# Performance work log

Measured on AMD Instinct MI355X. Metric: run time of the kernel, lower is better.

Reference implementation:

```python
import jax, jax.numpy as jnp
import numpy as np

N_HEADS = 16
ROPE_BASE = 10000.0


def setup_inputs() -> dict:
    key = jax.random.key(0)
    k1, k2, k3 = jax.random.split(key, 3)
    B, L, D = 2, 2048, 2048
    x = jax.random.normal(k1, (B, L, D), dtype=jnp.float32)
    w_qkv = jax.random.normal(k2, (D, 3 * D), dtype=jnp.float32) * (1.0 / np.sqrt(D))
    w_out = jax.random.normal(k3, (D, D), dtype=jnp.float32) * (1.0 / np.sqrt(D))
    return {"x": x, "w_qkv": w_qkv, "w_out": w_out}


def _rope_cos_sin(L, head_dim, dtype):
    # inv_freq over even dims, freqs duplicated across both halves (HF convention)
    inv_freq = 1.0 / (ROPE_BASE ** (jnp.arange(0, head_dim, 2, dtype=jnp.float32) / head_dim))
    freqs = jnp.arange(L, dtype=jnp.float32)[:, None] * inv_freq[None, :]  # [L, hd/2]
    emb = jnp.concatenate([freqs, freqs], axis=-1)  # [L, hd]
    return jnp.cos(emb).astype(dtype), jnp.sin(emb).astype(dtype)


def _rotate_half(t):
    h = t.shape[-1] // 2
    return jnp.concatenate([-t[..., h:], t[..., :h]], axis=-1)


def reference(x, w_qkv, w_out):
    B, L, D = x.shape
    H = N_HEADS
    hd = D // H
    qkv = x @ w_qkv  # [B, L, 3D]
    q, k, v = jnp.split(qkv, 3, axis=-1)

    def heads(t):  # [B, L, D] -> [B, H, L, hd]
        return t.reshape(B, L, H, hd).transpose(0, 2, 1, 3)

    q, k, v = heads(q), heads(k), heads(v)
    cos, sin = _rope_cos_sin(L, hd, x.dtype)  # [L, hd] broadcast over B,H
    q = q * cos + _rotate_half(q) * sin
    k = k * cos + _rotate_half(k) * sin
    # SDPA, no mask, no dropout (eval), not causal
    scale = 1.0 / np.sqrt(hd)
    scores = jnp.einsum('bhld,bhsd->bhls', q, k) * scale
    attn = jax.nn.softmax(scores, axis=-1)
    y = jnp.einsum('bhls,bhsd->bhld', attn, v)  # [B, H, L, hd]
    y = y.transpose(0, 2, 1, 3).reshape(B, L, D)
    return y @ w_out
```

## Files before the change

kernel.cpp:

```cpp
#include <hip/hip_runtime.h>

typedef __attribute__((ext_vector_type(8))) short bf16x8;
typedef __attribute__((ext_vector_type(8))) unsigned short u16x8;
typedef __attribute__((ext_vector_type(4))) float f32x4;
typedef __attribute__((ext_vector_type(4))) unsigned short u16x4;

#define BB 2
#define LL 2048
#define DD 2048
#define HH 16
#define HDIM 128
#define MM 4096
#define NQKV 6144

__device__ __forceinline__ unsigned short f2bf(float f) {
    unsigned int u = __builtin_bit_cast(unsigned int, f);
    u += 0x7FFFu + ((u >> 16) & 1u);
    return (unsigned short)(u >> 16);
}
__device__ __forceinline__ float bf2f(unsigned short h) {
    unsigned int u = ((unsigned int)h) << 16;
    return __builtin_bit_cast(float, u);
}

__device__ __forceinline__ void gload16(const unsigned short* g, unsigned short* l) {
    __builtin_amdgcn_global_load_lds((const __attribute__((address_space(1))) void*)g,
                                     (__attribute__((address_space(3))) void*)l, 16, 0, 0);
}

__global__ __launch_bounds__(256) void k_cvt_bf16(const float* __restrict__ in,
                                                  unsigned short* __restrict__ out,
                                                  int n4) {
    int i = blockIdx.x * 256 + threadIdx.x;
    if (i < n4) {
        float4 v = reinterpret_cast<const float4*>(in)[i];
        u16x4 o;
        o[0] = f2bf(v.x); o[1] = f2bf(v.y); o[2] = f2bf(v.z); o[3] = f2bf(v.w);
        reinterpret_cast<u16x4*>(out)[i] = o;
    }
}

__global__ __launch_bounds__(256) void k_cvt_T(const float* __restrict__ in,
                                               unsigned short* __restrict__ out,
                                               int K, int N) {
    __shared__ unsigned short t[64][72];
    int n0 = blockIdx.x * 64, k0 = blockIdx.y * 64;
    int tid = threadIdx.x;
    int tr = tid >> 4, tc = tid & 15;
    #pragma unroll
    for (int i = 0; i < 4; ++i) {
        int k = i * 16 + tr;
        float4 v = *reinterpret_cast<const float4*>(in + (size_t)(k0 + k) * N + n0 + tc * 4);
        t[tc * 4 + 0][k] = f2bf(v.x);
        t[tc * 4 + 1][k] = f2bf(v.y);
        t[tc * 4 + 2][k] = f2bf(v.z);
        t[tc * 4 + 3][k] = f2bf(v.w);
    }
    __syncthreads();
    #pragma unroll
    for (int i = 0; i < 4; ++i) {
        int n = i * 16 + tr;
        u16x4 o = *reinterpret_cast<u16x4*>(&t[n][tc * 4]);
        *reinterpret_cast<u16x4*>(out + (size_t)(n0 + n) * K + k0 + tc * 4) = o;
    }
}

__global__ __launch_bounds__(256) void k_transV(const unsigned short* __restrict__ in,
                                                unsigned short* __restrict__ out) {
    __shared__ unsigned short t[64][68];
    int l0 = blockIdx.x * 64, d0 = blockIdx.y * 64;
    int bh = blockIdx.z;
    const unsigned short* ib = in + (size_t)bh * LL * HDIM;
    unsigned short* ob = out + (size_t)bh * HDIM * LL;
    int tid = threadIdx.x;
    int tr = tid >> 4, tc = tid & 15;
    #pragma unroll
    for (int i = 0; i < 4; ++i) {
        int l = i * 16 + tr;
        u16x4 v = *reinterpret_cast<const u16x4*>(ib + (size_t)(l0 + l) * HDIM + d0 + tc * 4);
        t[tc * 4 + 0][l] = v[0];
        t[tc * 4 + 1][l] = v[1];
        t[tc * 4 + 2][l] = v[2];
        t[tc * 4 + 3][l] = v[3];
    }
    __syncthreads();
    #pragma unroll
    for (int i = 0; i < 4; ++i) {
        int d = i * 16 + tr;
        u16x4 o = *reinterpret_cast<u16x4*>(&t[d][tc * 4]);
        *reinterpret_cast<u16x4*>(ob + (size_t)(d0 + d) * LL + l0 + tc * 4) = o;
    }
}

__global__ __launch_bounds__(256) void k_rope_table(float* __restrict__ ct,
                                                    float* __restrict__ st) {
    int idx = blockIdx.x * 256 + threadIdx.x;
    if (idx >= LL * 64) return;
    int pos = idx >> 6, d = idx & 63;
    float freq = __expf(-(float)d * (9.210340371976184f / 64.0f));
    float ang = (float)pos * freq;
    ct[idx] = cosf(ang);
    st[idx] = sinf(ang);
}

__global__ __launch_bounds__(256) void k_rope_apply(unsigned short* __restrict__ Q,
                                                    unsigned short* __restrict__ K,
                                                    const float* __restrict__ ct,
                                                    const float* __restrict__ st) {
    int idx = blockIdx.x * 256 + threadIdx.x;
    int d = idx & 63;
    int pos = (idx >> 6) & (LL - 1);
    int bh = idx >> 17;
    size_t base = ((size_t)bh * LL + pos) * HDIM;
    float c = ct[pos * 64 + d], s = st[pos * 64 + d];
    float q0 = bf2f(Q[base + d]), q1 = bf2f(Q[base + d + 64]);
    Q[base + d]      = f2bf(q0 * c - q1 * s);
    Q[base + d + 64] = f2bf(q1 * c + q0 * s);
    float k0 = bf2f(K[base + d]), k1 = bf2f(K[base + d + 64]);
    K[base + d]      = f2bf(k0 * c - k1 * s);
    K[base + d + 64] = f2bf(k1 * c + k0 * s);
}

template<int EPI>
__global__ __launch_bounds__(256) void k_gemm8(const unsigned short* __restrict__ A,
                                               const unsigned short* __restrict__ Bt,
                                               int Nn, int Kn,
                                               unsigned short* __restrict__ outQ,
                                               unsigned short* __restrict__ outK,
                                               unsigned short* __restrict__ outV,
                                               float* __restrict__ outC) {
    __shared__ unsigned short sm[4 * 8192];
    const int tid = threadIdx.x;
    const int lane = tid & 63, w = tid >> 6;
    const int wm = w >> 1, wn = w & 1;
    const int lrow = lane & 15, lgrp = lane >> 4;
    const int m0 = blockIdx.y * 128, n0 = blockIdx.x * 128;
    const int NT = Kn / 32;

    const int srow = lane >> 2, scol = lane & 3;
    const int scolg = ((scol ^ ((srow >> 1) & 3)) * 8);
    const int fcol  = ((lgrp ^ ((lrow >> 1) & 3)) * 8);

    f32x4 acc[4][4] = {};

    auto stage = [&](int t) {
        const int kb = t * 32;
        unsigned short* buf = sm + (t & 3) * 8192;
        #pragma unroll
        for (int i = 0; i < 2; ++i) {
            int row = i * 64 + w * 16 + srow;
            gload16(A  + (size_t)(m0 + row) * Kn + kb + scolg, buf + i * 2048 + w * 512);
            gload16(Bt + (size_t)(n0 + row) * Kn + kb + scolg, buf + 4096 + i * 2048 + w * 512);
        }
    };

    auto tile_body = [&](int t, bool do_stage) {
        unsigned short* buf = sm + (t & 3) * 8192;
        bf16x8 af[4], bfr[4];
        #pragma unroll
        for (int f = 0; f < 4; ++f)
            af[f] = *reinterpret_cast<const bf16x8*>(buf + (wm * 64 + f * 16 + lrow) * 32 + fcol);
        #pragma unroll
        for (int f = 0; f < 4; ++f)
            bfr[f] = *reinterpret_cast<const bf16x8*>(buf + 4096 + (wn * 64 + f * 16 + lrow) * 32 + fcol);
        if (do_stage) stage(t + 3);
        __builtin_amdgcn_s_barrier();
        __builtin_amdgcn_s_setprio(1);
        #pragma unroll
        for (int fm = 0; fm < 4; ++fm)
            #pragma unroll
            for (int fn = 0; fn < 4; ++fn)
                acc[fm][fn] = __builtin_amdgcn_mfma_f32_16x16x32_bf16(af[fm], bfr[fn], acc[fm][fn], 0, 0, 0);
        __builtin_amdgcn_s_setprio(0);
    };

    stage(0); stage(1); stage(2);
    asm volatile("s_waitcnt vmcnt(8)" ::: "memory");
    __builtin_amdgcn_s_barrier();

    for (int t = 0; t < NT - 3; ++t) {
        tile_body(t, true);
        asm volatile("s_waitcnt vmcnt(8)" ::: "memory");
        __builtin_amdgcn_s_barrier();
    }
    tile_body(NT - 3, false);
    asm volatile("s_waitcnt vmcnt(4)" ::: "memory");
    __builtin_amdgcn_s_barrier();
    tile_body(NT - 2, false);
    asm volatile("s_waitcnt vmcnt(0)" ::: "memory");
    __builtin_amdgcn_s_barrier();
    tile_body(NT - 1, false);

    #pragma unroll
    for (int fm = 0; fm < 4; ++fm) {
        int mrow = m0 + wm * 64 + fm * 16 + lgrp * 4;
        #pragma unroll
        for (int fn = 0; fn < 4; ++fn) {
            int ncol = n0 + wn * 64 + fn * 16 + lrow;
            #pragma unroll
            for (int i = 0; i < 4; ++i) {
                float v = acc[fm][fn][i];
                int m = mrow + i;
                if constexpr (EPI == 0) {
                    int which = ncol >> 11;
                    int rr = ncol & (DD - 1);
                    int h = rr >> 7, d = rr & (HDIM - 1);
                    int b = m >> 11, pos = m & (LL - 1);
                    unsigned short* dst = (which == 0) ? outQ : ((which == 1) ? outK : outV);
                    dst[((size_t)(b * HH + h) * LL + pos) * HDIM + d] = f2bf(v);
                } else {
                    outC[(size_t)m * (size_t)Nn + ncol] = v;
                }
            }
        }
    }
}

__global__ __launch_bounds__(256, 2) void k_attn(const unsigned short* __restrict__ Q,
                                                 const unsigned short* __restrict__ K,
                                                 const unsigned short* __restrict__ Vt,
                                                 unsigned short* __restrict__ Y) {
    __shared__ unsigned short Kl[64][136];
    __shared__ unsigned short VTl[128][72];
    __shared__ unsigned short Pl[128][72];
    int tid = threadIdx.x;
    int lane = tid & 63, w = tid >> 6;
    int lrow = lane & 15, lgrp = lane >> 4;
    int orig = blockIdx.x;
    int id = (orig & 7) * 64 + (orig >> 3);
    int bh = id >> 4, qt = id & 15;
    int b = bh >> 4, h = bh & 15;
    const unsigned short* Qb = Q  + (size_t)bh * LL * HDIM;
    const unsigned short* Kb = K  + (size_t)bh * LL * HDIM;
    const unsigned short* Vb = Vt + (size_t)bh * HDIM * LL;
    int q0 = qt * 128 + w * 32;

    bf16x8 qf[2][4];
    #pragma unroll
    for (int rm = 0; rm < 2; ++rm)
        #pragma unroll
        for (int kk = 0; kk < 4; ++kk)
            qf[rm][kk] = *reinterpret_cast<const bf16x8*>(
                Qb + (size_t)(q0 + rm * 16 + lrow) * HDIM + kk * 32 + lgrp * 8);

    f32x4 accO[2][8] = {};
    f32x4 accL[2] = {};
    bf16x8 ones;
    #pragma unroll
    for (int j = 0; j < 8; ++j) ones[j] = (short)0x3F80;
    const float scale = 0.08838834764831845f;

    u16x8 kr[4], vr[4];
    auto sload = [&](int kt) {
        #pragma unroll
        for (int i = 0; i < 4; ++i) {
            int c = i * 256 + tid;
            kr[i] = *reinterpret_cast<const u16x8*>(Kb + (size_t)(kt * 64 + (c >> 4)) * HDIM + (c & 15) * 8);
            vr[i] = *reinterpret_cast<const u16x8*>(Vb + (size_t)(c >> 3) * LL + kt * 64 + (c & 7) * 8);
        }
    };
    auto swrite = [&]() {
        #pragma unroll
        for (int i = 0; i < 4; ++i) {
            int c = i * 256 + tid;
            *reinterpret_cast<u16x8*>(&Kl[c >> 4][(c & 15) * 8]) = kr[i];
            *reinterpret_cast<u16x8*>(&VTl[c >> 3][(c & 7) * 8]) = vr[i];
        }
    };

    sload(0);
    swrite();
    __syncthreads();

    for (int kt = 0; kt < LL / 64; ++kt) {
        if (kt + 1 < LL / 64) sload(kt + 1);

        f32x4 s[2][4] = {};
        __builtin_amdgcn_s_setprio(1);
        #pragma unroll
        for (int kn = 0; kn < 4; ++kn) {
            #pragma unroll
            for (int kk = 0; kk < 4; ++kk) {
                bf16x8 kf = *reinterpret_cast<const bf16x8*>(&Kl[kn * 16 + lrow][kk * 32 + lgrp * 8]);
                #pragma unroll
                for (int rm = 0; rm < 2; ++rm)
                    s[rm][kn] = __builtin_amdgcn_mfma_f32_16x16x32_bf16(qf[rm][kk], kf, s[rm][kn], 0, 0, 0);
            }
        }
        __builtin_amdgcn_s_setprio(0);

        #pragma unroll
        for (int rm = 0; rm < 2; ++rm)
            #pragma unroll
            for (int kn = 0; kn < 4; ++kn)
                #pragma unroll
                for (int i = 0; i < 4; ++i) {
                    float p = __expf(s[rm][kn][i] * scale);
                    Pl[w * 32 + rm * 16 + lgrp * 4 + i][kn * 16 + lrow] = f2bf(p);
                }

        __builtin_amdgcn_s_setprio(1);
        #pragma unroll
        for (int ks = 0; ks < 2; ++ks) {
            bf16x8 pa[2];
            #pragma unroll
            for (int rm = 0; rm < 2; ++rm) {
                pa[rm] = *reinterpret_cast<const bf16x8*>(&Pl[w * 32 + rm * 16 + lrow][ks * 32 + lgrp * 8]);
                accL[rm] = __builtin_amdgcn_mfma_f32_16x16x32_bf16(pa[rm], ones, accL[rm], 0, 0, 0);
            }
            #pragma unroll
            for (int dn = 0; dn < 8; ++dn) {
                bf16x8 vf = *reinterpret_cast<const bf16x8*>(&VTl[dn * 16 + lrow][ks * 32 + lgrp * 8]);
                #pragma unroll
                for (int rm = 0; rm < 2; ++rm)
                    accO[rm][dn] = __builtin_amdgcn_mfma_f32_16x16x32_bf16(pa[rm], vf, accO[rm][dn], 0, 0, 0);
            }
        }
        __builtin_amdgcn_s_setprio(0);

        __syncthreads();
        if (kt + 1 < LL / 64) {
            swrite();
            __syncthreads();
        }
    }

    #pragma unroll
    for (int rm = 0; rm < 2; ++rm)
        #pragma unroll
        for (int i = 0; i < 4; ++i) {
            float inv = 1.0f / accL[rm][i];
            int pos = q0 + rm * 16 + lgrp * 4 + i;
            #pragma unroll
            for (int dn = 0; dn < 8; ++dn) {
                int d = dn * 16 + lrow;
                Y[((size_t)b * LL + pos) * DD + h * HDIM + d] = f2bf(accO[rm][dn][i] * inv);
            }
        }
}

extern "C" void kernel_launch(void* const* d_in, const int* in_sizes, int n_in,
                              void* d_out, int out_size, void* d_ws, size_t ws_size,
                              hipStream_t stream) {
    const float* x     = (const float*)d_in[0];
    const float* wqkv  = (const float*)d_in[1];
    const float* wout  = (const float*)d_in[2];
    float* out = (float*)d_out;

    char* ws = (char*)d_ws;
    size_t off = 0;
    auto take = [&](size_t bytes) { char* p = ws + off; off += (bytes + 255) & ~(size_t)255; return p; };
    unsigned short* xb    = (unsigned short*)take((size_t)MM * DD * 2);
    unsigned short* wqkvT = (unsigned short*)take((size_t)DD * NQKV * 2);
    unsigned short* woutT = (unsigned short*)take((size_t)DD * DD * 2);
    unsigned short* Qb    = (unsigned short*)take((size_t)BB * HH * LL * HDIM * 2);
    unsigned short* Kb    = (unsigned short*)take((size_t)BB * HH * LL * HDIM * 2);
    unsigned short* Vb    = (unsigned short*)take((size_t)BB * HH * LL * HDIM * 2);
    unsigned short* Yb    = (unsigned short*)take((size_t)MM * DD * 2);
    float* ct             = (float*)take((size_t)LL * 64 * 4);
    float* st             = (float*)take((size_t)LL * 64 * 4);
    if (off > ws_size) return;
    unsigned short* VtB = xb;

    k_cvt_bf16<<<(MM * DD / 4 + 255) / 256, 256, 0, stream>>>(x, xb, MM * DD / 4);
    k_cvt_T<<<dim3(NQKV / 64, DD / 64), 256, 0, stream>>>(wqkv, wqkvT, DD, NQKV);
    k_cvt_T<<<dim3(DD / 64, DD / 64), 256, 0, stream>>>(wout, woutT, DD, DD);
    k_rope_table<<<(LL * 64 + 255) / 256, 256, 0, stream>>>(ct, st);

    k_gemm8<0><<<dim3(NQKV / 128, MM / 128), 256, 0, stream>>>(xb, wqkvT, NQKV, DD, Qb, Kb, Vb, nullptr);
    k_transV<<<dim3(LL / 64, HDIM / 64, BB * HH), 256, 0, stream>>>(Vb, VtB);
    k_rope_apply<<<(BB * HH * LL * 64) / 256, 256, 0, stream>>>(Qb, Kb, ct, st);
    k_attn<<<BB * HH * (LL / 128), 256, 0, stream>>>(Qb, Kb, VtB, Yb);
    k_gemm8<1><<<dim3(DD / 128, MM / 128), 256, 0, stream>>>(Yb, woutT, DD, DD, nullptr, nullptr, nullptr, out);
}
```

Measured before the change: 291.4 us.

## Use 256x256 tiles with 512 threads for QKV GEMM and XCD-aware block remap

The QKV projection GEMM moves to a new kernel with 256x256 output tiles, 8 waves, a 128 KB LDS ring buffer with a new XOR swizzle, and global-load staging split into two halves interleaved with two MFMA phases. Both GEMMs also remap the 1D block index so that consecutive tiles go to the same XCD (orig&7 striding), which should improve L2 reuse. Larger tiles raise arithmetic intensity per LDS byte. The costs are fewer blocks (384), higher register pressure from the 8x4 accumulators, and heavy LDS use that limits occupancy.

```diff
diff --git a/kernel.cpp b/kernel.cpp
--- a/kernel.cpp
+++ b/kernel.cpp
@@ -122,48 +122,62 @@
 }
 
 template<int EPI>
-__global__ __launch_bounds__(256) void k_gemm8(const unsigned short* __restrict__ A,
-                                               const unsigned short* __restrict__ Bt,
-                                               int Nn, int Kn,
-                                               unsigned short* __restrict__ outQ,
-                                               unsigned short* __restrict__ outK,
-                                               unsigned short* __restrict__ outV,
-                                               float* __restrict__ outC) {
-    __shared__ unsigned short sm[4 * 8192];
+__global__ __launch_bounds__(512) void k_gemm256(const unsigned short* __restrict__ A,
+                                                 const unsigned short* __restrict__ Bt,
+                                                 int Nn, int Kn,
+                                                 unsigned short* __restrict__ outQ,
+                                                 unsigned short* __restrict__ outK,
+                                                 unsigned short* __restrict__ outV,
+                                                 float* __restrict__ outC) {
+    __shared__ unsigned short sm[4 * 16384];
     const int tid = threadIdx.x;
     const int lane = tid & 63, w = tid >> 6;
-    const int wm = w >> 1, wn = w & 1;
+    const int wm = w >> 2, wn = w & 3;
     const int lrow = lane & 15, lgrp = lane >> 4;
-    const int m0 = blockIdx.y * 128, n0 = blockIdx.x * 128;
     const int NT = Kn / 32;
 
-    const int srow = lane >> 2, scol = lane & 3;
-    const int scolg = ((scol ^ ((srow >> 1) & 3)) * 8);
-    const int fcol  = ((lgrp ^ ((lrow >> 1) & 3)) * 8);
-
-    f32x4 acc[4][4] = {};
-
-    auto stage = [&](int t) {
+    int ntiles = 16 * (Nn >> 8);
+    int cpx = ntiles >> 3;
+    int orig = blockIdx.x;
+    int tau = (orig & 7) * cpx + (orig >> 3);
+    const int m0 = (tau & 15) * 256, n0 = (tau >> 4) * 256;
+
+    const int ssl = (lane & 7) ^ ((lane >> 3) & 7);
+    const int sRb = ((lane >> 3) << 1) + (ssl >> 2);
+    const int se  = (ssl & 3) * 8;
+
+    f32x4 acc[8][4] = {};
+
+    auto stage_part = [&](int t, int half) {
         const int kb = t * 32;
-        unsigned short* buf = sm + (t & 3) * 8192;
-        #pragma unroll
-        for (int i = 0; i < 2; ++i) {
-            int row = i * 64 + w * 16 + srow;
-            gload16(A  + (size_t)(m0 + row) * Kn + kb + scolg, buf + i * 2048 + w * 512);
-            gload16(Bt + (size_t)(n0 + row) * Kn + kb + scolg, buf + 4096 + i * 2048 + w * 512);
-        }
-    };
-
-    auto tile_body = [&](int t, bool do_stage) {
-        unsigned short* buf = sm + (t & 3) * 8192;
+        unsigned short* buf = sm + (t & 3) * 16384;
+        int R = (half * 8 + w) * 16 + sRb;
+        gload16(A  + (size_t)(m0 + R) * Kn + kb + se, buf + (half * 8 + w) * 512);
+        gload16(Bt + (size_t)(n0 + R) * Kn + kb + se, buf + 8192 + (half * 8 + w) * 512);
+    };
+
+    auto read_a = [&](unsigned short* buf, int fmBase, bf16x8* af) {
+        #pragma unroll
+        for (int f = 0; f < 4; ++f) {
+            int Rm = wm * 128 + (fmBase + f) * 16 + lrow;
+            int mr = Rm >> 1;
+            int sl = (((Rm & 1) << 2) | lgrp) ^ (mr & 7);
+            af[f] = *reinterpret_cast<const bf16x8*>(buf + mr * 64 + sl * 8);
+        }
+    };
+
+    auto tile_body = [&](int t, bool doStage) {
+        unsigned short* buf = sm + (t & 3) * 16384;
         bf16x8 af[4], bfr[4];
         #pragma unroll
-        for (int f = 0; f < 4; ++f)
-            af[f] = *reinterpret_cast<const bf16x8*>(buf + (wm * 64 + f * 16 + lrow) * 32 + fcol);
-        #pragma unroll
-        for (int f = 0; f < 4; ++f)
-            bfr[f] = *reinterpret_cast<const bf16x8*>(buf + 4096 + (wn * 64 + f * 16 + lrow) * 32 + fcol);
-        if (do_stage) stage(t + 3);
+        for (int f = 0; f < 4; ++f) {
+            int Rn = wn * 64 + f * 16 + lrow;
+            int mr = Rn >> 1;
+            int sl = (((Rn & 1) << 2) | lgrp) ^ (mr & 7);
+            bfr[f] = *reinterpret_cast<const bf16x8*>(buf + 8192 + mr * 64 + sl * 8);
+        }
+        read_a(buf, 0, af);
+        if (doStage) stage_part(t + 3, 0);
         __builtin_amdgcn_s_barrier();
         __builtin_amdgcn_s_setprio(1);
         #pragma unroll
@@ -172,9 +186,21 @@
             for (int fn = 0; fn < 4; ++fn)
                 acc[fm][fn] = __builtin_amdgcn_mfma_f32_16x16x32_bf16(af[fm], bfr[fn], acc[fm][fn], 0, 0, 0);
         __builtin_amdgcn_s_setprio(0);
-    };
-
-    stage(0); stage(1); stage(2);
+        read_a(buf, 4, af);
+        if (doStage) stage_part(t + 3, 1);
+        __builtin_amdgcn_s_barrier();
+        __builtin_amdgcn_s_setprio(1);
+        #pragma unroll
+        for (int fm = 0; fm < 4; ++fm)
+            #pragma unroll
+            for (int fn = 0; fn < 4; ++fn)
+                acc[4 + fm][fn] = __builtin_amdgcn_mfma_f32_16x16x32_bf16(af[fm], bfr[fn], acc[4 + fm][fn], 0, 0, 0);
+        __builtin_amdgcn_s_setprio(0);
+    };
+
+    stage_part(0, 0); stage_part(0, 1);
+    stage_part(1, 0); stage_part(1, 1);
+    stage_part(2, 0); stage_part(2, 1);
     asm volatile("s_waitcnt vmcnt(8)" ::: "memory");
     __builtin_amdgcn_s_barrier();
 
@@ -192,8 +218,8 @@
     tile_body(NT - 1, false);
 
     #pragma unroll
-    for (int fm = 0; fm < 4; ++fm) {
-        int mrow = m0 + wm * 64 + fm * 16 + lgrp * 4;
+    for (int fm = 0; fm < 8; ++fm) {
+        int mrow = m0 + wm * 128 + fm * 16 + lgrp * 4;
         #pragma unroll
         for (int fn = 0; fn < 4; ++fn) {
             int ncol = n0 + wn * 64 + fn * 16 + lrow;
@@ -212,6 +238,90 @@
                     outC[(size_t)m * (size_t)Nn + ncol] = v;
                 }
             }
+        }
+    }
+}
+
+template<int EPI>
+__global__ __launch_bounds__(256) void k_gemm8(const unsigned short* __restrict__ A,
+                                               const unsigned short* __restrict__ Bt,
+                                               int Nn, int Kn,
+                                               float* __restrict__ outC) {
+    __shared__ unsigned short sm[4 * 8192];
+    const int tid = threadIdx.x;
+    const int lane = tid & 63, w = tid >> 6;
+    const int wm = w >> 1, wn = w & 1;
+    const int lrow = lane & 15, lgrp = lane >> 4;
+    int ntiles = 32 * (Nn >> 7);
+    int cpx = ntiles >> 3;
+    int orig = blockIdx.x;
+    int tau = (orig & 7) * cpx + (orig >> 3);
+    const int m0 = (tau & 31) * 128, n0 = (tau >> 5) * 128;
+    const int NT = Kn / 32;
+
+    const int srow = lane >> 2, scol = lane & 3;
+    const int scolg = ((scol ^ ((srow >> 1) & 3)) * 8);
+    const int fcol  = ((lgrp ^ ((lrow >> 1) & 3)) * 8);
+
+    f32x4 acc[4][4] = {};
+
+    auto stage = [&](int t) {
+        const int kb = t * 32;
+        unsigned short* buf = sm + (t & 3) * 8192;
+        #pragma unroll
+        for (int i = 0; i < 2; ++i) {
+            int row = i * 64 + w * 16 + srow;
+            gload16(A  + (size_t)(m0 + row) * Kn + kb + scolg, buf + i * 2048 + w * 512);
+            gload16(Bt + (size_t)(n0 + row) * Kn + kb + scolg, buf + 4096 + i * 2048 + w * 512);
+        }
+    };
+
+    auto tile_body = [&](int t, bool do_stage) {
+        unsigned short* buf = sm + (t & 3) * 8192;
+        bf16x8 af[4], bfr[4];
+        #pragma unroll
+        for (int f = 0; f < 4; ++f)
+            af[f] = *reinterpret_cast<const bf16x8*>(buf + (wm * 64 + f * 16 + lrow) * 32 + fcol);
+        #pragma unroll
+        for (int f = 0; f < 4; ++f)
+            bfr[f] = *reinterpret_cast<const bf16x8*>(buf + 4096 + (wn * 64 + f * 16 + lrow) * 32 + fcol);
+        if (do_stage) stage(t + 3);
+        __builtin_amdgcn_s_barrier();
+        __builtin_amdgcn_s_setprio(1);
+        #pragma unroll
+        for (int fm = 0; fm < 4; ++fm)
+            #pragma unroll
+            for (int fn = 0; fn < 4; ++fn)
+                acc[fm][fn] = __builtin_amdgcn_mfma_f32_16x16x32_bf16(af[fm], bfr[fn], acc[fm][fn], 0, 0, 0);
+        __builtin_amdgcn_s_setprio(0);
+    };
+
+    stage(0); stage(1); stage(2);
+    asm volatile("s_waitcnt vmcnt(8)" ::: "memory");
+    __builtin_amdgcn_s_barrier();
+
+    for (int t = 0; t < NT - 3; ++t) {
+        tile_body(t, true);
+        asm volatile("s_waitcnt vmcnt(8)" ::: "memory");
+        __builtin_amdgcn_s_barrier();
+    }
+    tile_body(NT - 3, false);
+    asm volatile("s_waitcnt vmcnt(4)" ::: "memory");
+    __builtin_amdgcn_s_barrier();
+    tile_body(NT - 2, false);
+    asm volatile("s_waitcnt vmcnt(0)" ::: "memory");
+    __builtin_amdgcn_s_barrier();
+    tile_body(NT - 1, false);
+
+    #pragma unroll
+    for (int fm = 0; fm < 4; ++fm) {
+        int mrow = m0 + wm * 64 + fm * 16 + lgrp * 4;
+        #pragma unroll
+        for (int fn = 0; fn < 4; ++fn) {
+            int ncol = n0 + wn * 64 + fn * 16 + lrow;
+            #pragma unroll
+            for (int i = 0; i < 4; ++i)
+                outC[(size_t)(mrow + i) * (size_t)Nn + ncol] = acc[fm][fn][i];
         }
     }
 }
@@ -367,9 +477,9 @@
     k_cvt_T<<<dim3(DD / 64, DD / 64), 256, 0, stream>>>(wout, woutT, DD, DD);
     k_rope_table<<<(LL * 64 + 255) / 256, 256, 0, stream>>>(ct, st);
 
-    k_gemm8<0><<<dim3(NQKV / 128, MM / 128), 256, 0, stream>>>(xb, wqkvT, NQKV, DD, Qb, Kb, Vb, nullptr);
+    k_gemm256<0><<<16 * (NQKV / 256), 512, 0, stream>>>(xb, wqkvT, NQKV, DD, Qb, Kb, Vb, nullptr);
     k_transV<<<dim3(LL / 64, HDIM / 64, BB * HH), 256, 0, stream>>>(Vb, VtB);
     k_rope_apply<<<(BB * HH * LL * 64) / 256, 256, 0, stream>>>(Qb, Kb, ct, st);
     k_attn<<<BB * HH * (LL / 128), 256, 0, stream>>>(Qb, Kb, VtB, Yb);
-    k_gemm8<1><<<dim3(DD / 128, MM / 128), 256, 0, stream>>>(Yb, woutT, DD, DD, nullptr, nullptr, nullptr, out);
-}
+    k_gemm8<1><<<32 * (DD / 128), 256, 0, stream>>>(Yb, woutT, DD, DD, out);
+}
```

Result: slower. 302.0 us (+3.6%).

## Use 256x384 macro-tile GEMM with 512 threads for QKV projection

Applied to the files above, without the earlier changes.

Replaces the 128x128-tile QKV projection GEMM with a dedicated kernel that has 8 waves, a 256x384 output tile, a 3-stage LDS pipeline with staggered global loads, and an XCD-aware block remap. The launch is exactly 256 blocks, one per CU. The larger tile raises arithmetic intensity and cuts global/LDS traffic per FLOP, and the remap aims to improve L2 locality. In exchange it uses more registers (48 accumulators per thread) and more LDS, which may limit occupancy. The output GEMM template is simplified into a plain fp32 store kernel.

```diff
diff --git a/kernel.cpp b/kernel.cpp
--- a/kernel.cpp
+++ b/kernel.cpp
@@ -121,13 +121,118 @@
     K[base + d + 64] = f2bf(k1 * c + k0 * s);
 }
 
-template<int EPI>
+__global__ __launch_bounds__(512, 2) void k_gemm384(const unsigned short* __restrict__ A,
+                                                    const unsigned short* __restrict__ Bt,
+                                                    unsigned short* __restrict__ outQ,
+                                                    unsigned short* __restrict__ outK,
+                                                    unsigned short* __restrict__ outV) {
+    __shared__ unsigned short sm[3 * 20480];
+    const int Kn = DD;
+    const int tid = threadIdx.x;
+    const int lane = tid & 63, w = tid >> 6;
+    const int wm = w >> 2, wn = w & 3;
+    const int lrow = lane & 15, lgrp = lane >> 4;
+    const int NT = Kn / 32;
+
+    int orig = blockIdx.x;
+    int tau = (orig & 7) * 32 + (orig >> 3);
+    const int m0 = (tau & 15) * 256, n0 = (tau >> 4) * 384;
+
+    const int srow = lane >> 2, scol = lane & 3;
+    const int scolg = ((scol ^ ((srow >> 1) & 3)) * 8);
+    const int fcol  = ((lgrp ^ ((lrow >> 1) & 3)) * 8);
+
+    f32x4 acc[8][6] = {};
+
+    auto stageA = [&](int t, int r) {
+        unsigned short* dst = sm + (t % 3) * 20480 + (r * 128 + w * 16) * 32;
+        gload16(A + (size_t)(m0 + r * 128 + w * 16 + srow) * Kn + t * 32 + scolg, dst);
+    };
+    auto stageB = [&](int t, int r) {
+        unsigned short* dst = sm + (t % 3) * 20480 + 8192 + (r * 128 + w * 16) * 32;
+        gload16(Bt + (size_t)(n0 + r * 128 + w * 16 + srow) * Kn + t * 32 + scolg, dst);
+    };
+
+    auto body = [&](int t, bool doStage) {
+        unsigned short* bufA = sm + (t % 3) * 20480;
+        unsigned short* bufB = bufA + 8192;
+        bf16x8 af[8], bfr[2];
+        #pragma unroll
+        for (int f = 0; f < 8; ++f)
+            af[f] = *reinterpret_cast<const bf16x8*>(bufA + (wm * 128 + f * 16 + lrow) * 32 + fcol);
+        bfr[0] = *reinterpret_cast<const bf16x8*>(bufB + (wn * 96 + 0 * 16 + lrow) * 32 + fcol);
+        bfr[1] = *reinterpret_cast<const bf16x8*>(bufB + (wn * 96 + 1 * 16 + lrow) * 32 + fcol);
+        if (doStage) { stageA(t + 2, 0); stageA(t + 2, 1); }
+        __builtin_amdgcn_s_barrier();
+        __builtin_amdgcn_s_setprio(1);
+        #pragma unroll
+        for (int fm = 0; fm < 8; ++fm)
+            #pragma unroll
+            for (int j = 0; j < 2; ++j)
+                acc[fm][j] = __builtin_amdgcn_mfma_f32_16x16x32_bf16(af[fm], bfr[j], acc[fm][j], 0, 0, 0);
+        __builtin_amdgcn_s_setprio(0);
+        bfr[0] = *reinterpret_cast<const bf16x8*>(bufB + (wn * 96 + 2 * 16 + lrow) * 32 + fcol);
+        bfr[1] = *reinterpret_cast<const bf16x8*>(bufB + (wn * 96 + 3 * 16 + lrow) * 32 + fcol);
+        if (doStage) { stageB(t + 2, 0); stageB(t + 2, 1); }
+        __builtin_amdgcn_s_barrier();
+        __builtin_amdgcn_s_setprio(1);
+        #pragma unroll
+        for (int fm = 0; fm < 8; ++fm)
+            #pragma unroll
+            for (int j = 0; j < 2; ++j)
+                acc[fm][2 + j] = __builtin_amdgcn_mfma_f32_16x16x32_bf16(af[fm], bfr[j], acc[fm][2 + j], 0, 0, 0);
+        __builtin_amdgcn_s_setprio(0);
+        bfr[0] = *reinterpret_cast<const bf16x8*>(bufB + (wn * 96 + 4 * 16 + lrow) * 32 + fcol);
+        bfr[1] = *reinterpret_cast<const bf16x8*>(bufB + (wn * 96 + 5 * 16 + lrow) * 32 + fcol);
+        if (doStage) { stageB(t + 2, 2); }
+        __builtin_amdgcn_s_barrier();
+        __builtin_amdgcn_s_setprio(1);
+        #pragma unroll
+        for (int fm = 0; fm < 8; ++fm)
+            #pragma unroll
+            for (int j = 0; j < 2; ++j)
+                acc[fm][4 + j] = __builtin_amdgcn_mfma_f32_16x16x32_bf16(af[fm], bfr[j], acc[fm][4 + j], 0, 0, 0);
+        __builtin_amdgcn_s_setprio(0);
+    };
+
+    stageA(0, 0); stageA(0, 1); stageB(0, 0); stageB(0, 1); stageB(0, 2);
+    stageA(1, 0); stageA(1, 1); stageB(1, 0); stageB(1, 1); stageB(1, 2);
+    asm volatile("s_waitcnt vmcnt(5)" ::: "memory");
+    __builtin_amdgcn_s_barrier();
+
+    for (int t = 0; t < NT - 2; ++t) {
+        body(t, true);
+        asm volatile("s_waitcnt vmcnt(5)" ::: "memory");
+        __builtin_amdgcn_s_barrier();
+    }
+    body(NT - 2, false);
+    asm volatile("s_waitcnt vmcnt(0)" ::: "memory");
+    __builtin_amdgcn_s_barrier();
+    body(NT - 1, false);
+
+    #pragma unroll
+    for (int fm = 0; fm < 8; ++fm) {
+        int mrow = m0 + wm * 128 + fm * 16 + lgrp * 4;
+        #pragma unroll
+        for (int fn = 0; fn < 6; ++fn) {
+            int ncol = n0 + wn * 96 + fn * 16 + lrow;
+            int which = ncol >> 11;
+            int rr = ncol & (DD - 1);
+            int h = rr >> 7, d = rr & (HDIM - 1);
+            unsigned short* dst = (which == 0) ? outQ : ((which == 1) ? outK : outV);
+            #pragma unroll
+            for (int i = 0; i < 4; ++i) {
+                int m = mrow + i;
+                int b = m >> 11, pos = m & (LL - 1);
+                dst[((size_t)(b * HH + h) * LL + pos) * HDIM + d] = f2bf(acc[fm][fn][i]);
+            }
+        }
+    }
+}
+
 __global__ __launch_bounds__(256) void k_gemm8(const unsigned short* __restrict__ A,
                                                const unsigned short* __restrict__ Bt,
                                                int Nn, int Kn,
-                                               unsigned short* __restrict__ outQ,
-                                               unsigned short* __restrict__ outK,
-                                               unsigned short* __restrict__ outV,
                                                float* __restrict__ outC) {
     __shared__ unsigned short sm[4 * 8192];
     const int tid = threadIdx.x;
@@ -198,20 +303,8 @@
         for (int fn = 0; fn < 4; ++fn) {
             int ncol = n0 + wn * 64 + fn * 16 + lrow;
             #pragma unroll
-            for (int i = 0; i < 4; ++i) {
-                float v = acc[fm][fn][i];
-                int m = mrow + i;
-                if constexpr (EPI == 0) {
-                    int which = ncol >> 11;
-                    int rr = ncol & (DD - 1);
-                    int h = rr >> 7, d = rr & (HDIM - 1);
-                    int b = m >> 11, pos = m & (LL - 1);
-                    unsigned short* dst = (which == 0) ? outQ : ((which == 1) ? outK : outV);
-                    dst[((size_t)(b * HH + h) * LL + pos) * HDIM + d] = f2bf(v);
-                } else {
-                    outC[(size_t)m * (size_t)Nn + ncol] = v;
-                }
-            }
+            for (int i = 0; i < 4; ++i)
+                outC[(size_t)(mrow + i) * (size_t)Nn + ncol] = acc[fm][fn][i];
         }
     }
 }
@@ -367,9 +460,9 @@
     k_cvt_T<<<dim3(DD / 64, DD / 64), 256, 0, stream>>>(wout, woutT, DD, DD);
     k_rope_table<<<(LL * 64 + 255) / 256, 256, 0, stream>>>(ct, st);
 
-    k_gemm8<0><<<dim3(NQKV / 128, MM / 128), 256, 0, stream>>>(xb, wqkvT, NQKV, DD, Qb, Kb, Vb, nullptr);
+    k_gemm384<<<256, 512, 0, stream>>>(xb, wqkvT, Qb, Kb, Vb);
     k_transV<<<dim3(LL / 64, HDIM / 64, BB * HH), 256, 0, stream>>>(Vb, VtB);
     k_rope_apply<<<(BB * HH * LL * 64) / 256, 256, 0, stream>>>(Qb, Kb, ct, st);
     k_attn<<<BB * HH * (LL / 128), 256, 0, stream>>>(Qb, Kb, VtB, Yb);
-    k_gemm8<1><<<dim3(DD / 128, MM / 128), 256, 0, stream>>>(Yb, woutT, DD, DD, nullptr, nullptr, nullptr, out);
-}
+    k_gemm8<<<dim3(DD / 128, MM / 128), 256, 0, stream>>>(Yb, woutT, DD, DD, out);
+}
```

Result: faster. 269.4 us (-7.6%).
